# Optimization experiments

Hardware: AMD Instinct MI355X
Metric: run time of the kernel (lower is better)

Reference implementation:

```python
import jax, jax.numpy as jnp
import numpy as np

NUM_HEADS = 8
DIM = 256
NUM_Q = 1


def setup_inputs() -> dict:
    key = jax.random.key(0)
    ks = jax.random.split(key, 10)
    B, H, W, C = 4, 56, 56, DIM
    mask_h = mask_w = 7
    WinNum = mask_h * mask_w
    x = jax.random.normal(ks[0], (B, H, W, C), dtype=jnp.float32)
    clstoken = jax.random.normal(ks[1], (B, NUM_Q, C), dtype=jnp.float32)
    mask = jax.random.bernoulli(ks[2], 0.3, (B, WinNum, WinNum))
    # ensure each window attends to itself (avoid fully-masked rows)
    eye = jnp.eye(WinNum, dtype=bool)[None]
    mask = jnp.logical_or(mask, eye)
    Wqkv = jax.random.normal(ks[3], (C, 3 * C), dtype=jnp.float32) * (C ** -0.5)
    bqkv = jnp.zeros((3 * C,), dtype=jnp.float32)
    Wo = jax.random.normal(ks[4], (C, C), dtype=jnp.float32) * (C ** -0.5)
    bo = jnp.zeros((C,), dtype=jnp.float32)
    lepe_k = jax.random.normal(ks[5], (3, 3, 1, C), dtype=jnp.float32) * 0.1  # depthwise HWIO
    lepe_b = jnp.zeros((C,), dtype=jnp.float32)
    return {"x": x, "clstoken": clstoken, "mask": mask, "mask_h": mask_h,
            "mask_w": mask_w, "Wqkv": Wqkv, "bqkv": bqkv, "Wo": Wo, "bo": bo,
            "lepe_k": lepe_k, "lepe_b": lepe_b}


def _forward(x, clstoken, mask, mask_h, mask_w, Wqkv, bqkv, Wo, bo, lepe_k, lepe_b):
    B, H, W, C = x.shape
    num_q = clstoken.shape[1]
    Nh = NUM_HEADS
    Hd = C // Nh
    Win_h, Win_w = H // mask_h, W // mask_w
    WinPix = Win_h * Win_w
    WinNum = mask_h * mask_w
    L_win = H * W
    scale = C ** -0.5

    qkv = x @ Wqkv + bqkv                       # [B,H,W,3C]
    q, k, v = jnp.split(qkv, 3, axis=-1)
    qkv_cls = clstoken @ Wqkv + bqkv            # [B,Q,3C]
    q_cls, k_cls, v_cls = jnp.split(qkv_cls, 3, axis=-1)

    # depthwise lepe conv on v (NHWC)
    lepe = jax.lax.conv_general_dilated(
        v, lepe_k, window_strides=(1, 1), padding='SAME',
        dimension_numbers=('NHWC', 'HWIO', 'NHWC'), feature_group_count=C) + lepe_b

    def to_win(t):  # b (j h)(i w)(Nh Hd) -> b Nh (j i h w) Hd
        t = t.reshape(B, mask_h, Win_h, mask_w, Win_w, Nh, Hd)
        t = t.transpose(0, 5, 1, 3, 2, 4, 6)
        return t.reshape(B, Nh, L_win, Hd)

    def cls_heads(t):  # b q (Nh Hd) -> b Nh q Hd
        return t.reshape(B, num_q, Nh, Hd).transpose(0, 2, 1, 3)

    q_all = jnp.concatenate([to_win(q), cls_heads(q_cls)], axis=2)
    k_all = jnp.concatenate([to_win(k), cls_heads(k_cls)], axis=2)
    v_all = jnp.concatenate([to_win(v), cls_heads(v_cls)], axis=2)

    # token-level block mask; cls block (id WinNum) is globally visible
    blk = jnp.concatenate([jnp.arange(L_win) // WinPix,
                           jnp.full((num_q,), WinNum)])
    mask_ext = jnp.pad(mask, ((0, 0), (0, 1), (0, 1)), constant_values=True)
    tok_mask = mask_ext[:, blk[:, None], blk[None, :]]  # [B,L,L]

    scores = jnp.einsum('bnqd,bnkd->bnqk', q_all, k_all) * scale
    neg = jnp.finfo(scores.dtype).min
    scores = jnp.where(tok_mask[:, None], scores, neg)
    attn = jax.nn.softmax(scores, axis=-1)
    out = jnp.einsum('bnqk,bnkd->bnqd', attn, v_all)   # [B,Nh,L,Hd]

    cls_out = out[:, :, -num_q:, :]
    x_out = out[:, :, :-num_q, :]
    # b Nh (j i h w) Hd -> b (j h)(i w)(Nh Hd)
    x_out = x_out.reshape(B, Nh, mask_h, mask_w, Win_h, Win_w, Hd)
    x_out = x_out.transpose(0, 2, 4, 3, 5, 1, 6).reshape(B, H, W, C)
    cls_out = cls_out.transpose(0, 2, 1, 3).reshape(B, num_q, C)

    x_out = (x_out + lepe) @ Wo + bo
    cls_out = cls_out @ Wo + bo
    return x_out, cls_out


def reference(x, clstoken, mask, mask_h, mask_w, Wqkv, bqkv, Wo, bo, lepe_k, lepe_b):
    return _forward(x, clstoken, mask, mask_h, mask_w, Wqkv, bqkv, Wo, bo, lepe_k, lepe_b)
```

## Files before the change

kernel.cpp:

```cpp
#include <hip/hip_runtime.h>
#include <math.h>

#define B_      4
#define NH      8
#define HD      32
#define WINNUM  49
#define LWIN    3136
#define NTOK    3137
#define NPIX    12544
#define MROWS   12548
#define SCALE_L2E 0.09016844005556021f
#define SM_BIAS   4.0f

typedef _Float16 half_t;
using half8 = __attribute__((ext_vector_type(8))) half_t;
using half4 = __attribute__((ext_vector_type(4))) half_t;
using f32x4 = __attribute__((ext_vector_type(4))) float;

__device__ __forceinline__ unsigned pack2(float a, float b) {
    auto h = __builtin_amdgcn_cvt_pkrtz(a, b);
    return __builtin_bit_cast(unsigned, h);
}
__device__ __forceinline__ half8 as_h8(int4 v) {
    return __builtin_bit_cast(half8, v);
}

__global__ __launch_bounds__(256)
void prep(const float* __restrict__ x, const float* __restrict__ cls,
          const float* __restrict__ Wqkv, const float* __restrict__ Wo,
          half_t* __restrict__ xh, half_t* __restrict__ Wqkvt, half_t* __restrict__ Wot)
{
    const int idx = blockIdx.x * 256 + threadIdx.x;
    const int stride = gridDim.x * 256;
    for (int i = idx; i < MROWS * 256; i += stride) {
        int row = i >> 8, c = i & 255;
        float v = (row < NPIX) ? x[i] : cls[(row - NPIX) * 256 + c];
        xh[i] = (half_t)v;
    }
    for (int i = idx; i < 768 * 256; i += stride) {
        int n = i >> 8, k = i & 255;
        Wqkvt[i] = (half_t)Wqkv[k * 768 + n];
    }
    for (int i = idx; i < 256 * 256; i += stride) {
        int n = i >> 8, k = i & 255;
        Wot[i] = (half_t)Wo[k * 256 + n];
    }
}

__global__ __launch_bounds__(256)
void qkv_gemm(const half_t* __restrict__ xh, const half_t* __restrict__ Bt,
              const float* __restrict__ bqkv,
              half_t* __restrict__ qh, half_t* __restrict__ kh,
              half_t* __restrict__ khcls, half_t* __restrict__ vh,
              half_t* __restrict__ vplain)
{
    __shared__ __align__(16) short As[2][128 * 40];
    __shared__ __align__(16) short Bs[2][128 * 40];
    const int m0 = blockIdx.y * 128, n0 = blockIdx.x * 128;
    const int tid = threadIdx.x;
    const int lane = tid & 63, wv = tid >> 6;
    const int wm = wv >> 1, wn = wv & 1;
    const int qi = lane & 15, g = lane >> 4;
    f32x4 acc[4][4] = {};

    int4 ra[2], rb[2];
    auto issue = [&](int k0) {
#pragma unroll
        for (int i = 0; i < 2; ++i) {
            int ch = tid + 256 * i;
            int row = ch >> 2, kc = (ch & 3) * 8;
            int m = m0 + row;
            ra[i] = (m < MROWS) ? *(const int4*)(xh + (size_t)m * 256 + k0 + kc)
                                : make_int4(0, 0, 0, 0);
            rb[i] = *(const int4*)(Bt + (size_t)(n0 + row) * 256 + k0 + kc);
        }
    };
    auto commit = [&](int bu) {
#pragma unroll
        for (int i = 0; i < 2; ++i) {
            int ch = tid + 256 * i;
            int row = ch >> 2, kc = (ch & 3) * 8;
            *(int4*)&As[bu][row * 40 + kc] = ra[i];
            *(int4*)&Bs[bu][row * 40 + kc] = rb[i];
        }
    };

    issue(0); commit(0);
    __syncthreads();
    int buf = 0;
    for (int s = 0; s < 8; ++s) {
        if (s < 7) issue((s + 1) * 32);
        half8 af[4], bf[4];
#pragma unroll
        for (int f = 0; f < 4; ++f) {
            af[f] = *(const half8*)&As[buf][(wm * 64 + f * 16 + qi) * 40 + g * 8];
            bf[f] = *(const half8*)&Bs[buf][(wn * 64 + f * 16 + qi) * 40 + g * 8];
        }
#pragma unroll
        for (int fm = 0; fm < 4; ++fm)
#pragma unroll
            for (int fn = 0; fn < 4; ++fn)
                acc[fm][fn] = __builtin_amdgcn_mfma_f32_16x16x32_f16(af[fm], bf[fn], acc[fm][fn], 0, 0, 0);
        if (s < 7) commit(buf ^ 1);
        __syncthreads();
        buf ^= 1;
    }

    const int part = n0 >> 8;
    int nhv[4], dv[4];
    float bq[4];
#pragma unroll
    for (int fn = 0; fn < 4; ++fn) {
        int n = n0 + wn * 64 + fn * 16 + qi;
        bq[fn] = bqkv[n];
        int c = n & 255;
        nhv[fn] = c >> 5; dv[fn] = c & 31;
    }
#pragma unroll
    for (int fm = 0; fm < 4; ++fm) {
#pragma unroll
        for (int r = 0; r < 4; ++r) {
            int m = m0 + wm * 64 + fm * 16 + g * 4 + r;
            if (m >= MROWS) continue;
            int b, tok;
            if (m < NPIX) {
                b = m / LWIN;
                int p = m - b * LWIN;
                int hh = p / 56, ww = p - hh * 56;
                tok = ((hh >> 3) * 7 + (ww >> 3)) * 64 + ((hh & 7) << 3) + (ww & 7);
            } else { b = m - NPIX; tok = LWIN; }
#pragma unroll
            for (int fn = 0; fn < 4; ++fn) {
                float val = acc[fm][fn][r] + bq[fn];
                size_t bh = (size_t)(b * NH + nhv[fn]);
                int d = dv[fn];
                if (part == 0) {
                    qh[(bh * NTOK + tok) * 32 + d] = (half_t)(val * SCALE_L2E);
                } else if (part == 1) {
                    if (tok < LWIN) kh[(bh * WINNUM + (tok >> 6)) * 2560 + (tok & 63) * 40 + d] = (half_t)val;
                    else            khcls[bh * 32 + d] = (half_t)val;
                } else {
                    vplain[(bh * NTOK + tok) * 32 + d] = (half_t)val;
                    if (tok < LWIN) vh[(bh * WINNUM + (tok >> 6)) * 2560 + d * 80 + (tok & 63)] = (half_t)val;
                }
            }
        }
    }
}

__global__ __launch_bounds__(256)
void win_attn(const half_t* __restrict__ qh, const half_t* __restrict__ kh,
              const half_t* __restrict__ khcls, const half_t* __restrict__ vh,
              const half_t* __restrict__ vplain, const int* __restrict__ mask,
              half_t* __restrict__ tg, float* __restrict__ clspart)
{
    const int id = blockIdx.x;
    const int tid = threadIdx.x;
    __shared__ __align__(16) short Plds[4][16 * 72];
    __shared__ float redc[4 * 33];
    const int lane = tid & 63, wv = tid >> 6;

    if (id >= 1568) {
        const int cid = id - 1568;
        const int bh = cid >> 3;
        const int chunk = cid & 7;
        const int wstart = chunk * 6;
        const int nw = (chunk < 7) ? 6 : 7;
        const int nkeys = nw * 64;

        float q[32];
        {
            const half_t* qp = qh + ((size_t)bh * NTOK + LWIN) * 32;
#pragma unroll
            for (int d = 0; d < 32; ++d) q[d] = (float)qp[d];
        }
        float l = 0.f, o[32];
#pragma unroll
        for (int d = 0; d < 32; ++d) o[d] = 0.f;

        const half_t* kwb = kh + (size_t)bh * (WINNUM * 2560) + wstart * 2560;
        const half_t* vb  = vplain + ((size_t)bh * NTOK + wstart * 64) * 32;

        for (int kk = tid; kk < nkeys; kk += 256) {
            const half_t* kp = kwb + (kk >> 6) * 2560 + (kk & 63) * 40;
            float s = 0.f;
#pragma unroll
            for (int c8 = 0; c8 < 4; ++c8) {
                half8 kv = *(const half8*)(kp + c8 * 8);
#pragma unroll
                for (int j = 0; j < 8; ++j) s += q[c8 * 8 + j] * (float)kv[j];
            }
            float pp = exp2f(s - SM_BIAS);
            l += pp;
            const half_t* vp = vb + (size_t)kk * 32;
#pragma unroll
            for (int c8 = 0; c8 < 4; ++c8) {
                half8 vvv = *(const half8*)(vp + c8 * 8);
#pragma unroll
                for (int j = 0; j < 8; ++j) o[c8 * 8 + j] += pp * (float)vvv[j];
            }
        }
        if (chunk == 7 && tid == 0) {
            const half_t* kp = khcls + bh * 32;
            float s = 0.f;
#pragma unroll
            for (int d = 0; d < 32; ++d) s += q[d] * (float)kp[d];
            float pp = exp2f(s - SM_BIAS);
            l += pp;
            const half_t* vp = vplain + ((size_t)bh * NTOK + LWIN) * 32;
#pragma unroll
            for (int d = 0; d < 32; ++d) o[d] += pp * (float)vp[d];
        }
#pragma unroll
        for (int off = 1; off < 64; off <<= 1) {
            l += __shfl_xor(l, off);
#pragma unroll
            for (int d = 0; d < 32; ++d) o[d] += __shfl_xor(o[d], off);
        }
        if (lane == 0) {
#pragma unroll
            for (int d = 0; d < 32; ++d) redc[wv * 33 + d] = o[d];
            redc[wv * 33 + 32] = l;
        }
        __syncthreads();
        if (tid < 33) {
            float s = redc[tid] + redc[33 + tid] + redc[66 + tid] + redc[99 + tid];
            clspart[(bh * 8 + chunk) * 33 + tid] = s;
        }
        return;
    }

    const int sw = (id & 7) * 196 + (id >> 3);
    const int wi = sw % 49;
    const int bh = sw / 49;
    const int b = bh >> 3, nh = bh & 7;

    const int g = lane >> 4, qi = lane & 15;
    const int qrow = wi * 64 + wv * 16 + qi;

    half8 aq = *(const half8*)(qh + ((size_t)bh * NTOK + qrow) * 32 + g * 8);

    float lacc = 0.f;
    f32x4 acc[2] = {{0.f,0.f,0.f,0.f},{0.f,0.f,0.f,0.f}};

    const int* mrow = mask + (b * WINNUM + wi) * WINNUM;
    int mv = (lane < WINNUM) ? mrow[lane] : 0;
    unsigned long long rem = __ballot(mv != 0);

    const half_t* kwin = kh + (size_t)bh * (WINNUM * 2560);
    const half_t* vwin = vh + (size_t)bh * (WINNUM * 2560);
    const int koff = qi * 40 + g * 8;
    const int voff = qi * 80 + g * 8;

    short* pw = &Plds[wv][qi * 72];
    const short* prd = &Plds[wv][qi * 72 + g * 8];

    while (rem) {
        const int wj = __builtin_ctzll(rem);
        rem &= rem - 1;
        const half_t* kb = kwin + wj * 2560 + koff;
        const half_t* vb = vwin + wj * 2560 + voff;
        int4 kf0 = *(const int4*)(kb);
        int4 kf1 = *(const int4*)(kb + 640);
        int4 kf2 = *(const int4*)(kb + 1280);
        int4 kf3 = *(const int4*)(kb + 1920);
        int4 vf00 = *(const int4*)(vb);
        int4 vf01 = *(const int4*)(vb + 32);
        int4 vf10 = *(const int4*)(vb + 1280);
        int4 vf11 = *(const int4*)(vb + 1312);

        f32x4 st[4];
        __builtin_amdgcn_s_setprio(1);
        st[0] = __builtin_amdgcn_mfma_f32_16x16x32_f16(as_h8(kf0), aq, (f32x4){0.f,0.f,0.f,0.f}, 0, 0, 0);
        st[1] = __builtin_amdgcn_mfma_f32_16x16x32_f16(as_h8(kf1), aq, (f32x4){0.f,0.f,0.f,0.f}, 0, 0, 0);
        st[2] = __builtin_amdgcn_mfma_f32_16x16x32_f16(as_h8(kf2), aq, (f32x4){0.f,0.f,0.f,0.f}, 0, 0, 0);
        st[3] = __builtin_amdgcn_mfma_f32_16x16x32_f16(as_h8(kf3), aq, (f32x4){0.f,0.f,0.f,0.f}, 0, 0, 0);
        __builtin_amdgcn_s_setprio(0);

#pragma unroll
        for (int t = 0; t < 4; ++t) {
            float p0 = exp2f(st[t][0] - SM_BIAS);
            float p1 = exp2f(st[t][1] - SM_BIAS);
            float p2 = exp2f(st[t][2] - SM_BIAS);
            float p3 = exp2f(st[t][3] - SM_BIAS);
            lacc += (p0 + p1) + (p2 + p3);
            uint2 pk = make_uint2(pack2(p0, p1), pack2(p2, p3));
            *(uint2*)&pw[t * 16 + 4 * g] = pk;
        }
        half8 bp0 = *(const half8*)(prd);
        half8 bp1 = *(const half8*)(prd + 32);
        __builtin_amdgcn_s_setprio(1);
        acc[0] = __builtin_amdgcn_mfma_f32_16x16x32_f16(as_h8(vf00), bp0, acc[0], 0, 0, 0);
        acc[1] = __builtin_amdgcn_mfma_f32_16x16x32_f16(as_h8(vf10), bp0, acc[1], 0, 0, 0);
        acc[0] = __builtin_amdgcn_mfma_f32_16x16x32_f16(as_h8(vf01), bp1, acc[0], 0, 0, 0);
        acc[1] = __builtin_amdgcn_mfma_f32_16x16x32_f16(as_h8(vf11), bp1, acc[1], 0, 0, 0);
        __builtin_amdgcn_s_setprio(0);
    }

    lacc += __shfl_xor(lacc, 16);
    lacc += __shfl_xor(lacc, 32);

    float kcls[8], vcls[2][4];
#pragma unroll
    for (int j = 0; j < 8; ++j) kcls[j] = (float)khcls[bh * 32 + g * 8 + j];
    {
        const half_t* vcb = vplain + ((size_t)bh * NTOK + LWIN) * 32;
#pragma unroll
        for (int h2 = 0; h2 < 2; ++h2)
#pragma unroll
            for (int r = 0; r < 4; ++r) vcls[h2][r] = (float)vcb[h2 * 16 + g * 4 + r];
    }
    float sc = 0.f;
#pragma unroll
    for (int j = 0; j < 8; ++j) sc += (float)aq[j] * kcls[j];
    sc += __shfl_xor(sc, 16);
    sc += __shfl_xor(sc, 32);
    float pc = exp2f(sc - SM_BIAS);
    float l = lacc + pc;
#pragma unroll
    for (int h2 = 0; h2 < 2; ++h2)
#pragma unroll
        for (int r = 0; r < 4; ++r) acc[h2][r] += pc * vcls[h2][r];

    {
        float inv = 1.f / l;
        int kk = wv * 16 + qi;
        int hh = (wi / 7) * 8 + (kk >> 3);
        int ww = (wi % 7) * 8 + (kk & 7);
        size_t pix = (size_t)b * LWIN + hh * 56 + ww;
        half_t* tp = tg + pix * 256 + nh * 32;
#pragma unroll
        for (int h2 = 0; h2 < 2; ++h2) {
            half4 hv;
#pragma unroll
            for (int r = 0; r < 4; ++r) hv[r] = (half_t)(acc[h2][r] * inv);
            *(half4*)(tp + h2 * 16 + g * 4) = hv;
        }
    }
}

__global__ __launch_bounds__(256)
void lepe_add(const half_t* __restrict__ vplain, const float* __restrict__ lk,
              const float* __restrict__ lb, const float* __restrict__ clspart,
              half_t* __restrict__ tg)
{
    if (blockIdx.x == 1568) {
        const int c = threadIdx.x;
        const int nh = c >> 5, d = c & 31;
#pragma unroll
        for (int b = 0; b < 4; ++b) {
            int bh = b * NH + nh;
            float os = 0.f, ls = 0.f;
#pragma unroll
            for (int ch = 0; ch < 8; ++ch) {
                os += clspart[(bh * 8 + ch) * 33 + d];
                ls += clspart[(bh * 8 + ch) * 33 + 32];
            }
            tg[(size_t)(NPIX + b) * 256 + c] = (half_t)(os / ls);
        }
        return;
    }
    const int gidx = blockIdx.x * 256 + threadIdx.x;
    const int pix = gidx >> 5, cg = gidx & 31;
    const int c0 = cg * 8;
    const int b = pix / LWIN, p = pix - b * LWIN;
    const int hh = p / 56, ww = p - hh * 56;
    const int nh = c0 >> 5, d0 = c0 & 31;
    const half_t* vb = vplain + (size_t)(b * NH + nh) * NTOK * 32 + d0;

    float s[8];
#pragma unroll
    for (int j = 0; j < 8; ++j) s[j] = lb[c0 + j];
#pragma unroll
    for (int dh = -1; dh <= 1; ++dh) {
        int hn = hh + dh;
        if (hn < 0 || hn >= 56) continue;
#pragma unroll
        for (int dw = -1; dw <= 1; ++dw) {
            int wn = ww + dw;
            if (wn < 0 || wn >= 56) continue;
            int tok = ((hn >> 3) * 7 + (wn >> 3)) * 64 + ((hn & 7) << 3) + (wn & 7);
            half8 vvv = *(const half8*)(vb + (size_t)tok * 32);
            const float* kk = lk + ((dh + 1) * 3 + (dw + 1)) * 256 + c0;
#pragma unroll
            for (int j = 0; j < 8; ++j) s[j] += (float)vvv[j] * kk[j];
        }
    }
    half_t* tp = tg + (size_t)pix * 256 + c0;
    half8 cur = *(const half8*)tp;
    half8 outv;
#pragma unroll
    for (int j = 0; j < 8; ++j) outv[j] = (half_t)((float)cur[j] + s[j]);
    *(half8*)tp = outv;
}

__global__ __launch_bounds__(256)
void out_gemm(const half_t* __restrict__ th, const half_t* __restrict__ Bt,
              const float* __restrict__ bo, float* __restrict__ out)
{
    __shared__ __align__(16) short As[2][128 * 40];
    __shared__ __align__(16) short Bs[2][128 * 40];
    const int m0 = blockIdx.y * 128, n0 = blockIdx.x * 128;
    const int tid = threadIdx.x;
    const int lane = tid & 63, wv = tid >> 6;
    const int wm = wv >> 1, wn = wv & 1;
    const int qi = lane & 15, g = lane >> 4;
    f32x4 acc[4][4] = {};

    int4 ra[2], rb[2];
    auto issue = [&](int k0) {
#pragma unroll
        for (int i = 0; i < 2; ++i) {
            int ch = tid + 256 * i;
            int row = ch >> 2, kc = (ch & 3) * 8;
            int m = m0 + row;
            ra[i] = (m < MROWS) ? *(const int4*)(th + (size_t)m * 256 + k0 + kc)
                                : make_int4(0, 0, 0, 0);
            rb[i] = *(const int4*)(Bt + (size_t)(n0 + row) * 256 + k0 + kc);
        }
    };
    auto commit = [&](int bu) {
#pragma unroll
        for (int i = 0; i < 2; ++i) {
            int ch = tid + 256 * i;
            int row = ch >> 2, kc = (ch & 3) * 8;
            *(int4*)&As[bu][row * 40 + kc] = ra[i];
            *(int4*)&Bs[bu][row * 40 + kc] = rb[i];
        }
    };

    issue(0); commit(0);
    __syncthreads();
    int buf = 0;
    for (int s = 0; s < 8; ++s) {
        if (s < 7) issue((s + 1) * 32);
        half8 af[4], bf[4];
#pragma unroll
        for (int f = 0; f < 4; ++f) {
            af[f] = *(const half8*)&As[buf][(wm * 64 + f * 16 + qi) * 40 + g * 8];
            bf[f] = *(const half8*)&Bs[buf][(wn * 64 + f * 16 + qi) * 40 + g * 8];
        }
#pragma unroll
        for (int fm = 0; fm < 4; ++fm)
#pragma unroll
            for (int fn = 0; fn < 4; ++fn)
                acc[fm][fn] = __builtin_amdgcn_mfma_f32_16x16x32_f16(af[fm], bf[fn], acc[fm][fn], 0, 0, 0);
        if (s < 7) commit(buf ^ 1);
        __syncthreads();
        buf ^= 1;
    }

    float bov[4];
    int nn[4];
#pragma unroll
    for (int fn = 0; fn < 4; ++fn) {
        nn[fn] = n0 + wn * 64 + fn * 16 + qi;
        bov[fn] = bo[nn[fn]];
    }
#pragma unroll
    for (int fm = 0; fm < 4; ++fm)
#pragma unroll
        for (int r = 0; r < 4; ++r) {
            int m = m0 + wm * 64 + fm * 16 + g * 4 + r;
            if (m >= MROWS) continue;
#pragma unroll
            for (int fn = 0; fn < 4; ++fn)
                out[(size_t)m * 256 + nn[fn]] = acc[fm][fn][r] + bov[fn];
        }
}

extern "C" void kernel_launch(void* const* d_in, const int* in_sizes, int n_in,
                              void* d_out, int out_size, void* d_ws, size_t ws_size,
                              hipStream_t stream)
{
    const float* x    = (const float*)d_in[0];
    const float* cls  = (const float*)d_in[1];
    const int*   mask = (const int*)d_in[2];
    const float* Wqkv = (const float*)d_in[5];
    const float* bqkv = (const float*)d_in[6];
    const float* Wo   = (const float*)d_in[7];
    const float* bo   = (const float*)d_in[8];
    const float* lk   = (const float*)d_in[9];
    const float* lb   = (const float*)d_in[10];
    float* out = (float*)d_out;

    char* w = (char*)d_ws;
    half_t* xh     = (half_t*)w;  w += 6424576;
    half_t* qh     = (half_t*)w;  w += 6424576;
    half_t* kh     = (half_t*)w;  w += 8028160;
    half_t* khcls  = (half_t*)w;  w += 2048;
    half_t* vh     = (half_t*)w;  w += 8028160;
    half_t* vplain = (half_t*)w;  w += 6424576;
    half_t* Wqkvt  = (half_t*)w;  w += 393216;
    half_t* Wot    = (half_t*)w;  w += 131072;
    half_t* th     = (half_t*)w;  w += 6424576;
    float*  clspart= (float*)w;   w += 33792;

    prep<<<1600, 256, 0, stream>>>(x, cls, Wqkv, Wo, xh, Wqkvt, Wot);
    qkv_gemm<<<dim3(6, 99), 256, 0, stream>>>(xh, Wqkvt, bqkv, qh, kh, khcls, vh, vplain);
    win_attn<<<1824, 256, 0, stream>>>(qh, kh, khcls, vh, vplain, mask, th, clspart);
    lepe_add<<<1569, 256, 0, stream>>>(vplain, lk, lb, clspart, th);
    out_gemm<<<dim3(2, 99), 256, 0, stream>>>(th, Wot, bo, out);
}
```

Baseline: 122.1 us.

## Use 32x32 MFMA in window attention with ones-MFMA row sums; shrink out_gemm tile

The window attention kernel now runs two waves of 32 query rows each and uses 32x32x16 MFMA instructions in place of 16x16x32. The softmax denominator is computed by an extra MFMA against a ones matrix, replacing scalar accumulation and shuffles. The fixed exp bias is removed, which raises the risk of fp16 overflow in P if scores get large. out_gemm switches to 64-row M tiles so the grid doubles to improve CU occupancy, and the cls path adjusts for 128-thread blocks.

```diff
diff --git a/kernel.cpp b/kernel.cpp
--- a/kernel.cpp
+++ b/kernel.cpp
@@ -10,12 +10,12 @@
 #define NPIX    12544
 #define MROWS   12548
 #define SCALE_L2E 0.09016844005556021f
-#define SM_BIAS   4.0f
 
 typedef _Float16 half_t;
-using half8 = __attribute__((ext_vector_type(8))) half_t;
-using half4 = __attribute__((ext_vector_type(4))) half_t;
-using f32x4 = __attribute__((ext_vector_type(4))) float;
+using half8  = __attribute__((ext_vector_type(8))) half_t;
+using half4  = __attribute__((ext_vector_type(4))) half_t;
+using f32x4  = __attribute__((ext_vector_type(4))) float;
+using f32x16 = __attribute__((ext_vector_type(16))) float;
 
 __device__ __forceinline__ unsigned pack2(float a, float b) {
     auto h = __builtin_amdgcn_cvt_pkrtz(a, b);
@@ -148,7 +148,7 @@
     }
 }
 
-__global__ __launch_bounds__(256)
+__global__ __launch_bounds__(128)
 void win_attn(const half_t* __restrict__ qh, const half_t* __restrict__ kh,
               const half_t* __restrict__ khcls, const half_t* __restrict__ vh,
               const half_t* __restrict__ vplain, const int* __restrict__ mask,
@@ -156,8 +156,8 @@
 {
     const int id = blockIdx.x;
     const int tid = threadIdx.x;
-    __shared__ __align__(16) short Plds[4][16 * 72];
-    __shared__ float redc[4 * 33];
+    __shared__ __align__(16) short Plds[2][32 * 72];
+    __shared__ float redc[2 * 33];
     const int lane = tid & 63, wv = tid >> 6;
 
     if (id >= 1568) {
@@ -181,7 +181,7 @@
         const half_t* kwb = kh + (size_t)bh * (WINNUM * 2560) + wstart * 2560;
         const half_t* vb  = vplain + ((size_t)bh * NTOK + wstart * 64) * 32;
 
-        for (int kk = tid; kk < nkeys; kk += 256) {
+        for (int kk = tid; kk < nkeys; kk += 128) {
             const half_t* kp = kwb + (kk >> 6) * 2560 + (kk & 63) * 40;
             float s = 0.f;
 #pragma unroll
@@ -190,7 +190,7 @@
 #pragma unroll
                 for (int j = 0; j < 8; ++j) s += q[c8 * 8 + j] * (float)kv[j];
             }
-            float pp = exp2f(s - SM_BIAS);
+            float pp = exp2f(s);
             l += pp;
             const half_t* vp = vb + (size_t)kk * 32;
 #pragma unroll
@@ -205,7 +205,7 @@
             float s = 0.f;
 #pragma unroll
             for (int d = 0; d < 32; ++d) s += q[d] * (float)kp[d];
-            float pp = exp2f(s - SM_BIAS);
+            float pp = exp2f(s);
             l += pp;
             const half_t* vp = vplain + ((size_t)bh * NTOK + LWIN) * 32;
 #pragma unroll
@@ -224,8 +224,7 @@
         }
         __syncthreads();
         if (tid < 33) {
-            float s = redc[tid] + redc[33 + tid] + redc[66 + tid] + redc[99 + tid];
-            clspart[(bh * 8 + chunk) * 33 + tid] = s;
+            clspart[(bh * 8 + chunk) * 33 + tid] = redc[tid] + redc[33 + tid];
         }
         return;
     }
@@ -235,13 +234,23 @@
     const int bh = sw / 49;
     const int b = bh >> 3, nh = bh & 7;
 
-    const int g = lane >> 4, qi = lane & 15;
-    const int qrow = wi * 64 + wv * 16 + qi;
-
-    half8 aq = *(const half8*)(qh + ((size_t)bh * NTOK + qrow) * 32 + g * 8);
-
-    float lacc = 0.f;
-    f32x4 acc[2] = {{0.f,0.f,0.f,0.f},{0.f,0.f,0.f,0.f}};
+    const int qc = lane & 31;
+    const int hb = lane >> 5;
+    const int qbase = wi * 64 + wv * 32;
+
+    const half_t* qp = qh + ((size_t)bh * NTOK + qbase + qc) * 32 + hb * 8;
+    half8 aq0 = as_h8(*(const int4*)(qp));
+    half8 aq1 = as_h8(*(const int4*)(qp + 16));
+
+    half8 onesA = {};
+    if (qc == 0) {
+#pragma unroll
+        for (int j = 0; j < 8; ++j) onesA[j] = (half_t)1.0f;
+    }
+
+    const f32x16 Z16 = {0.f,0.f,0.f,0.f,0.f,0.f,0.f,0.f,0.f,0.f,0.f,0.f,0.f,0.f,0.f,0.f};
+    f32x16 acc   = Z16;
+    f32x16 acc_l = Z16;
 
     const int* mrow = mask + (b * WINNUM + wi) * WINNUM;
     int mv = (lane < WINNUM) ? mrow[lane] : 0;
@@ -249,92 +258,97 @@
 
     const half_t* kwin = kh + (size_t)bh * (WINNUM * 2560);
     const half_t* vwin = vh + (size_t)bh * (WINNUM * 2560);
-    const int koff = qi * 40 + g * 8;
-    const int voff = qi * 80 + g * 8;
-
-    short* pw = &Plds[wv][qi * 72];
-    const short* prd = &Plds[wv][qi * 72 + g * 8];
+
+    short* pw = &Plds[wv][qc * 72];
+    const short* prd = &Plds[wv][qc * 72 + hb * 8];
 
     while (rem) {
         const int wj = __builtin_ctzll(rem);
         rem &= rem - 1;
-        const half_t* kb = kwin + wj * 2560 + koff;
-        const half_t* vb = vwin + wj * 2560 + voff;
-        int4 kf0 = *(const int4*)(kb);
-        int4 kf1 = *(const int4*)(kb + 640);
-        int4 kf2 = *(const int4*)(kb + 1280);
-        int4 kf3 = *(const int4*)(kb + 1920);
-        int4 vf00 = *(const int4*)(vb);
-        int4 vf01 = *(const int4*)(vb + 32);
-        int4 vf10 = *(const int4*)(vb + 1280);
-        int4 vf11 = *(const int4*)(vb + 1312);
-
-        f32x4 st[4];
+        const half_t* kb = kwin + wj * 2560 + qc * 40 + hb * 8;
+        const half_t* vb = vwin + wj * 2560 + qc * 80 + hb * 8;
+        int4 kf00 = *(const int4*)(kb);
+        int4 kf01 = *(const int4*)(kb + 16);
+        int4 kf10 = *(const int4*)(kb + 1280);
+        int4 kf11 = *(const int4*)(kb + 1296);
+        int4 vf0 = *(const int4*)(vb);
+        int4 vf1 = *(const int4*)(vb + 16);
+        int4 vf2 = *(const int4*)(vb + 32);
+        int4 vf3 = *(const int4*)(vb + 48);
+
+        f32x16 st[2];
         __builtin_amdgcn_s_setprio(1);
-        st[0] = __builtin_amdgcn_mfma_f32_16x16x32_f16(as_h8(kf0), aq, (f32x4){0.f,0.f,0.f,0.f}, 0, 0, 0);
-        st[1] = __builtin_amdgcn_mfma_f32_16x16x32_f16(as_h8(kf1), aq, (f32x4){0.f,0.f,0.f,0.f}, 0, 0, 0);
-        st[2] = __builtin_amdgcn_mfma_f32_16x16x32_f16(as_h8(kf2), aq, (f32x4){0.f,0.f,0.f,0.f}, 0, 0, 0);
-        st[3] = __builtin_amdgcn_mfma_f32_16x16x32_f16(as_h8(kf3), aq, (f32x4){0.f,0.f,0.f,0.f}, 0, 0, 0);
+        st[0] = __builtin_amdgcn_mfma_f32_32x32x16_f16(as_h8(kf00), aq0, Z16, 0, 0, 0);
+        st[1] = __builtin_amdgcn_mfma_f32_32x32x16_f16(as_h8(kf10), aq0, Z16, 0, 0, 0);
+        st[0] = __builtin_amdgcn_mfma_f32_32x32x16_f16(as_h8(kf01), aq1, st[0], 0, 0, 0);
+        st[1] = __builtin_amdgcn_mfma_f32_32x32x16_f16(as_h8(kf11), aq1, st[1], 0, 0, 0);
         __builtin_amdgcn_s_setprio(0);
 
 #pragma unroll
-        for (int t = 0; t < 4; ++t) {
-            float p0 = exp2f(st[t][0] - SM_BIAS);
-            float p1 = exp2f(st[t][1] - SM_BIAS);
-            float p2 = exp2f(st[t][2] - SM_BIAS);
-            float p3 = exp2f(st[t][3] - SM_BIAS);
-            lacc += (p0 + p1) + (p2 + p3);
-            uint2 pk = make_uint2(pack2(p0, p1), pack2(p2, p3));
-            *(uint2*)&pw[t * 16 + 4 * g] = pk;
-        }
-        half8 bp0 = *(const half8*)(prd);
-        half8 bp1 = *(const half8*)(prd + 32);
+        for (int t = 0; t < 2; ++t)
+#pragma unroll
+            for (int rb = 0; rb < 4; ++rb) {
+                float p0 = exp2f(st[t][4 * rb + 0]);
+                float p1 = exp2f(st[t][4 * rb + 1]);
+                float p2 = exp2f(st[t][4 * rb + 2]);
+                float p3 = exp2f(st[t][4 * rb + 3]);
+                *(uint2*)&pw[t * 32 + 8 * rb + 4 * hb] =
+                    make_uint2(pack2(p0, p1), pack2(p2, p3));
+            }
+
+        half8 pB0 = *(const half8*)(prd);
+        half8 pB1 = *(const half8*)(prd + 16);
+        half8 pB2 = *(const half8*)(prd + 32);
+        half8 pB3 = *(const half8*)(prd + 48);
         __builtin_amdgcn_s_setprio(1);
-        acc[0] = __builtin_amdgcn_mfma_f32_16x16x32_f16(as_h8(vf00), bp0, acc[0], 0, 0, 0);
-        acc[1] = __builtin_amdgcn_mfma_f32_16x16x32_f16(as_h8(vf10), bp0, acc[1], 0, 0, 0);
-        acc[0] = __builtin_amdgcn_mfma_f32_16x16x32_f16(as_h8(vf01), bp1, acc[0], 0, 0, 0);
-        acc[1] = __builtin_amdgcn_mfma_f32_16x16x32_f16(as_h8(vf11), bp1, acc[1], 0, 0, 0);
+        acc   = __builtin_amdgcn_mfma_f32_32x32x16_f16(as_h8(vf0), pB0, acc, 0, 0, 0);
+        acc_l = __builtin_amdgcn_mfma_f32_32x32x16_f16(onesA, pB0, acc_l, 0, 0, 0);
+        acc   = __builtin_amdgcn_mfma_f32_32x32x16_f16(as_h8(vf1), pB1, acc, 0, 0, 0);
+        acc_l = __builtin_amdgcn_mfma_f32_32x32x16_f16(onesA, pB1, acc_l, 0, 0, 0);
+        acc   = __builtin_amdgcn_mfma_f32_32x32x16_f16(as_h8(vf2), pB2, acc, 0, 0, 0);
+        acc_l = __builtin_amdgcn_mfma_f32_32x32x16_f16(onesA, pB2, acc_l, 0, 0, 0);
+        acc   = __builtin_amdgcn_mfma_f32_32x32x16_f16(as_h8(vf3), pB3, acc, 0, 0, 0);
+        acc_l = __builtin_amdgcn_mfma_f32_32x32x16_f16(onesA, pB3, acc_l, 0, 0, 0);
         __builtin_amdgcn_s_setprio(0);
     }
 
-    lacc += __shfl_xor(lacc, 16);
-    lacc += __shfl_xor(lacc, 32);
-
-    float kcls[8], vcls[2][4];
-#pragma unroll
-    for (int j = 0; j < 8; ++j) kcls[j] = (float)khcls[bh * 32 + g * 8 + j];
+    float lwin = __shfl(acc_l[0], qc);
+
+    float sc = 0.f;
+    {
+        const half_t* kcb = khcls + bh * 32 + hb * 8;
+        half8 kc0 = *(const half8*)(kcb);
+        half8 kc1 = *(const half8*)(kcb + 16);
+#pragma unroll
+        for (int j = 0; j < 8; ++j)
+            sc += (float)aq0[j] * (float)kc0[j] + (float)aq1[j] * (float)kc1[j];
+        sc += __shfl_xor(sc, 32);
+    }
+    float pc = exp2f(sc);
+    float l = lwin + pc;
     {
         const half_t* vcb = vplain + ((size_t)bh * NTOK + LWIN) * 32;
 #pragma unroll
-        for (int h2 = 0; h2 < 2; ++h2)
-#pragma unroll
-            for (int r = 0; r < 4; ++r) vcls[h2][r] = (float)vcb[h2 * 16 + g * 4 + r];
-    }
-    float sc = 0.f;
-#pragma unroll
-    for (int j = 0; j < 8; ++j) sc += (float)aq[j] * kcls[j];
-    sc += __shfl_xor(sc, 16);
-    sc += __shfl_xor(sc, 32);
-    float pc = exp2f(sc - SM_BIAS);
-    float l = lacc + pc;
-#pragma unroll
-    for (int h2 = 0; h2 < 2; ++h2)
-#pragma unroll
-        for (int r = 0; r < 4; ++r) acc[h2][r] += pc * vcls[h2][r];
+        for (int rb = 0; rb < 4; ++rb) {
+            half4 vc = *(const half4*)(vcb + 8 * rb + 4 * hb);
+#pragma unroll
+            for (int r = 0; r < 4; ++r) acc[4 * rb + r] += pc * (float)vc[r];
+        }
+    }
 
     {
         float inv = 1.f / l;
-        int kk = wv * 16 + qi;
+        int kk = wv * 32 + qc;
         int hh = (wi / 7) * 8 + (kk >> 3);
         int ww = (wi % 7) * 8 + (kk & 7);
         size_t pix = (size_t)b * LWIN + hh * 56 + ww;
         half_t* tp = tg + pix * 256 + nh * 32;
 #pragma unroll
-        for (int h2 = 0; h2 < 2; ++h2) {
+        for (int rb = 0; rb < 4; ++rb) {
             half4 hv;
 #pragma unroll
-            for (int r = 0; r < 4; ++r) hv[r] = (half_t)(acc[h2][r] * inv);
-            *(half4*)(tp + h2 * 16 + g * 4) = hv;
+            for (int r = 0; r < 4; ++r) hv[r] = (half_t)(acc[4 * rb + r] * inv);
+            *(half4*)(tp + 8 * rb + 4 * hb) = hv;
         }
     }
 }
@@ -398,33 +412,39 @@
 void out_gemm(const half_t* __restrict__ th, const half_t* __restrict__ Bt,
               const float* __restrict__ bo, float* __restrict__ out)
 {
-    __shared__ __align__(16) short As[2][128 * 40];
+    __shared__ __align__(16) short As[2][64 * 40];
     __shared__ __align__(16) short Bs[2][128 * 40];
-    const int m0 = blockIdx.y * 128, n0 = blockIdx.x * 128;
+    const int m0 = blockIdx.y * 64, n0 = blockIdx.x * 128;
     const int tid = threadIdx.x;
     const int lane = tid & 63, wv = tid >> 6;
     const int wm = wv >> 1, wn = wv & 1;
     const int qi = lane & 15, g = lane >> 4;
-    f32x4 acc[4][4] = {};
-
-    int4 ra[2], rb[2];
+    f32x4 acc[2][4] = {};
+
+    int4 ra, rb[2];
     auto issue = [&](int k0) {
+        {
+            int row = tid >> 2, kc = (tid & 3) * 8;
+            int m = m0 + row;
+            ra = (m < MROWS) ? *(const int4*)(th + (size_t)m * 256 + k0 + kc)
+                             : make_int4(0, 0, 0, 0);
+        }
 #pragma unroll
         for (int i = 0; i < 2; ++i) {
             int ch = tid + 256 * i;
             int row = ch >> 2, kc = (ch & 3) * 8;
-            int m = m0 + row;
-            ra[i] = (m < MROWS) ? *(const int4*)(th + (size_t)m * 256 + k0 + kc)
-                                : make_int4(0, 0, 0, 0);
             rb[i] = *(const int4*)(Bt + (size_t)(n0 + row) * 256 + k0 + kc);
         }
     };
     auto commit = [&](int bu) {
+        {
+            int row = tid >> 2, kc = (tid & 3) * 8;
+            *(int4*)&As[bu][row * 40 + kc] = ra;
+        }
 #pragma unroll
         for (int i = 0; i < 2; ++i) {
             int ch = tid + 256 * i;
             int row = ch >> 2, kc = (ch & 3) * 8;
-            *(int4*)&As[bu][row * 40 + kc] = ra[i];
             *(int4*)&Bs[bu][row * 40 + kc] = rb[i];
         }
     };
@@ -434,14 +454,15 @@
     int buf = 0;
     for (int s = 0; s < 8; ++s) {
         if (s < 7) issue((s + 1) * 32);
-        half8 af[4], bf[4];
-#pragma unroll
-        for (int f = 0; f < 4; ++f) {
-            af[f] = *(const half8*)&As[buf][(wm * 64 + f * 16 + qi) * 40 + g * 8];
+        half8 af[2], bf[4];
+#pragma unroll
+        for (int f = 0; f < 2; ++f)
+            af[f] = *(const half8*)&As[buf][(wm * 32 + f * 16 + qi) * 40 + g * 8];
+#pragma unroll
+        for (int f = 0; f < 4; ++f)
             bf[f] = *(const half8*)&Bs[buf][(wn * 64 + f * 16 + qi) * 40 + g * 8];
-        }
-#pragma unroll
-        for (int fm = 0; fm < 4; ++fm)
+#pragma unroll
+        for (int fm = 0; fm < 2; ++fm)
 #pragma unroll
             for (int fn = 0; fn < 4; ++fn)
                 acc[fm][fn] = __builtin_amdgcn_mfma_f32_16x16x32_f16(af[fm], bf[fn], acc[fm][fn], 0, 0, 0);
@@ -458,10 +479,10 @@
         bov[fn] = bo[nn[fn]];
     }
 #pragma unroll
-    for (int fm = 0; fm < 4; ++fm)
+    for (int fm = 0; fm < 2; ++fm)
 #pragma unroll
         for (int r = 0; r < 4; ++r) {
-            int m = m0 + wm * 64 + fm * 16 + g * 4 + r;
+            int m = m0 + wm * 32 + fm * 16 + g * 4 + r;
             if (m >= MROWS) continue;
 #pragma unroll
             for (int fn = 0; fn < 4; ++fn)
@@ -498,7 +519,7 @@
 
     prep<<<1600, 256, 0, stream>>>(x, cls, Wqkv, Wo, xh, Wqkvt, Wot);
     qkv_gemm<<<dim3(6, 99), 256, 0, stream>>>(xh, Wqkvt, bqkv, qh, kh, khcls, vh, vplain);
-    win_attn<<<1824, 256, 0, stream>>>(qh, kh, khcls, vh, vplain, mask, th, clspart);
+    win_attn<<<1824, 128, 0, stream>>>(qh, kh, khcls, vh, vplain, mask, th, clspart);
     lepe_add<<<1569, 256, 0, stream>>>(vplain, lk, lb, clspart, th);
-    out_gemm<<<dim3(2, 99), 256, 0, stream>>>(th, Wot, bo, out);
-}
+    out_gemm<<<dim3(2, 197), 256, 0, stream>>>(th, Wot, bo, out);
+}
```

Result: slower. 125.2 us (+2.5%).
